# Kernel tuning notes

Measured on AMD Instinct MI355X. Metric: run time of the kernel, lower is better.

## Reference

```python
import jax, jax.numpy as jnp
import numpy as np

NEG = -9e8

def _leaky(x):
    return jax.nn.leaky_relu(x, 0.01)

def _gru(x, h, wih, whh, bih, bhh):
    # torch.nn.GRUCell math
    gi = x @ wih.T + bih
    gh = h @ whh.T + bhh
    ir, iz, inn = jnp.split(gi, 3, axis=-1)
    hr, hz, hn = jnp.split(gh, 3, axis=-1)
    r = jax.nn.sigmoid(ir + hr)
    z = jax.nn.sigmoid(iz + hz)
    n = jnp.tanh(inn + r * hn)
    return (1.0 - z) * n + z * h

def _gather(feat, idx):
    # feat [B,S,F], idx [B,S,K] -> [B,S,K,F]; -1 wraps to last row, masked later (same as torch)
    return jax.vmap(lambda f, i: f[i])(feat, idx)

def setup_inputs() -> dict:
    key = jax.random.key(0)
    ks = jax.random.split(key, 32)
    B, S, K, F_in, E, R = 32, 512, 21, 26, 256, 3
    amino_list = jax.random.uniform(ks[0], (B, S, F_in), dtype=jnp.float32)
    idx = jax.random.randint(ks[1], (B, S, K), 0, S, dtype=jnp.int32)
    pad = jax.random.uniform(ks[2], (B, S, K)) < 0.3
    amino_degree_list = jnp.where(pad, jnp.int32(-1), idx)
    # variable sequence lengths for mask
    lens = jax.random.randint(ks[3], (B,), S // 2, S + 1)
    amino_mask = (jnp.arange(S)[None, :] < lens[:, None]).astype(jnp.float32)
    s = 0.05
    d = dict(
        amino_list=amino_list,
        amino_degree_list=amino_degree_list,
        amino_mask=amino_mask,
        emb_W=jax.random.normal(ks[4], (E, F_in)) * s,
        emb_b=jax.random.normal(ks[5], (E,)) * s,
        neigh_W=jax.random.normal(ks[6], (E, F_in)) * s,
        neigh_b=jax.random.normal(ks[7], (E,)) * s,
        align_W=jax.random.normal(ks[8], (R, 1, 2 * E)) * s,
        align_b=jax.random.normal(ks[9], (R, 1)) * s,
        attend_W=jax.random.normal(ks[10], (R, E, E)) * s,
        attend_b=jax.random.normal(ks[11], (R, E)) * s,
        gru_wih=jax.random.normal(ks[12], (R, 3 * E, E)) * s,
        gru_whh=jax.random.normal(ks[13], (R, 3 * E, E)) * s,
        gru_bih=jax.random.normal(ks[14], (R, 3 * E)) * s,
        gru_bhh=jax.random.normal(ks[15], (R, 3 * E)) * s,
        seq_align_W=jax.random.normal(ks[16], (1, 2 * E)) * s,
        seq_align_b=jax.random.normal(ks[17], (1,)) * s,
        seq_attend_W=jax.random.normal(ks[18], (E, E)) * s,
        seq_attend_b=jax.random.normal(ks[19], (E,)) * s,
        sgru_wih=jax.random.normal(ks[20], (3 * E, E)) * s,
        sgru_whh=jax.random.normal(ks[21], (3 * E, E)) * s,
        sgru_bih=jax.random.normal(ks[22], (3 * E,)) * s,
        sgru_bhh=jax.random.normal(ks[23], (3 * E,)) * s,
    )
    return d

RADIUS = 3
T_STEPS = 2

def reference(amino_list, amino_degree_list, amino_mask,
              emb_W, emb_b, neigh_W, neigh_b,
              align_W, align_b, attend_W, attend_b,
              gru_wih, gru_whh, gru_bih, gru_bhh,
              seq_align_W, seq_align_b, seq_attend_W, seq_attend_b,
              sgru_wih, sgru_whh, sgru_bih, sgru_bhh):
    B, S, _ = amino_list.shape
    E = emb_W.shape[0]
    K = amino_degree_list.shape[-1]

    mask3 = amino_mask[:, :, None]                       # [B,S,1]
    amino_feature = _leaky(amino_list @ emb_W.T + emb_b)  # [B,S,E]

    attend_mask = (amino_degree_list != -1).astype(jnp.float32)[..., None]   # [B,S,K,1]
    softmax_mask = jnp.where(amino_degree_list == -1, NEG, 0.0)[..., None]   # [B,S,K,1]

    # first radius step: neighbors from raw one-hot features via neighbor_fc
    neighbor = _gather(amino_list, amino_degree_list)                 # [B,S,K,F_in]
    neighbor_feature = _leaky(neighbor @ neigh_W.T + neigh_b)         # [B,S,K,E]

    h = amino_feature.reshape(B * S, E)
    activated = None
    for d in range(RADIUS):
        if d == 0:
            nbr = neighbor_feature
            cur = amino_feature
        else:
            nbr = _gather(activated, amino_degree_list)               # [B,S,K,E]
            cur = activated
        cur_exp = jnp.broadcast_to(cur[:, :, None, :], (B, S, K, E))
        feat_align = jnp.concatenate([cur_exp, nbr], axis=-1)         # [B,S,K,2E]
        score = _leaky(feat_align @ align_W[d].T + align_b[d]) + softmax_mask
        attw = jax.nn.softmax(score, axis=-2) * attend_mask           # [B,S,K,1]
        nbr_t = nbr @ attend_W[d].T + attend_b[d]                     # [B,S,K,E]
        context = jax.nn.elu(jnp.sum(attw * nbr_t, axis=-2))          # [B,S,E]
        h = _gru(context.reshape(B * S, E), h, gru_wih[d], gru_whh[d], gru_bih[d], gru_bhh[d])
        activated = jax.nn.relu(h.reshape(B, S, E))

    seq_feature = jnp.sum(activated * mask3, axis=-2)                 # [B,E]
    act_mol = jax.nn.relu(seq_feature)
    seq_softmax_mask = jnp.where(mask3 == 0.0, NEG, 0.0)              # [B,S,1]

    act_seq = act_mol
    for _ in range(T_STEPS):
        mol_exp = jnp.broadcast_to(act_mol[:, None, :], (B, S, E))
        sa = jnp.concatenate([mol_exp, activated], axis=-1)           # [B,S,2E]
        score = _leaky(sa @ seq_align_W.T + seq_align_b) + seq_softmax_mask
        w = jax.nn.softmax(score, axis=-2) * mask3                    # [B,S,1]
        feat_t = activated @ seq_attend_W.T + seq_attend_b            # [B,S,E]
        seq_context = jax.nn.elu(jnp.sum(w * feat_t, axis=-2))        # [B,E]
        seq_feature = _gru(seq_context, seq_feature, sgru_wih, sgru_whh, sgru_bih, sgru_bhh)
        act_seq = jax.nn.relu(seq_feature)
    return act_seq
```

## Files before the change

kernel.cpp:

```cpp
#include <hip/hip_runtime.h>
#include <hip/hip_bf16.h>
#include <math.h>


#define NEGC (-9.0e8f)

typedef __attribute__((ext_vector_type(8))) short bf16x8;
typedef __attribute__((ext_vector_type(4))) float f32x4;

__device__ __forceinline__ ushort f2bf(float x) {
    union { float f; unsigned u; } v; v.f = x;
    unsigned r = v.u + 0x7FFF + ((v.u >> 16) & 1);
    return (ushort)(r >> 16);
}
__device__ __forceinline__ float bf2f(ushort u) {
    union { unsigned u; float f; } v; v.u = ((unsigned)u) << 16;
    return v.f;
}
__device__ __forceinline__ float sigm_fast(float x) {
    return 1.f / (1.f + __expf(-x));
}
__device__ __forceinline__ float tanh_fast(float x) {
    return 1.f - 2.f / (__expf(2.f * x) + 1.f);
}
__device__ __forceinline__ float elu_fast(float x) {
    return x > 0.f ? x : (__expf(x) - 1.f);
}

typedef const __attribute__((address_space(1))) void gvoid_t;
typedef __attribute__((address_space(3))) void lvoid_t;

__global__ __launch_bounds__(256) void cvt4_kernel(
    const float* __restrict__ s0, ushort* __restrict__ d0, int n0,
    const float* __restrict__ s1, ushort* __restrict__ d1, int n1,
    const float* __restrict__ s2, ushort* __restrict__ d2, int n2,
    const float* __restrict__ s3, ushort* __restrict__ d3, int n3)
{
    int i = blockIdx.x * 256 + threadIdx.x;
    const float* s; ushort* dst; int l;
    if (i < n0) { s = s0; dst = d0; l = i; }
    else if (i < n0 + n1) { s = s1; dst = d1; l = i - n0; }
    else if (i < n0 + n1 + n2) { s = s2; dst = d2; l = i - n0 - n1; }
    else if (i < n0 + n1 + n2 + n3) { s = s3; dst = d3; l = i - n0 - n1 - n2; }
    else return;
    float4 v = *reinterpret_cast<const float4*>(s + (size_t)l * 4);
    ushort4 o; o.x = f2bf(v.x); o.y = f2bf(v.y); o.z = f2bf(v.z); o.w = f2bf(v.w);
    *reinterpret_cast<ushort4*>(dst + (size_t)l * 4) = o;
}

__global__ __launch_bounds__(256) void gemm_dual_kernel(
    const ushort* __restrict__ A0, const ushort* __restrict__ W0,
    const float* __restrict__ b0, ushort* __restrict__ C0, int n0t,
    const ushort* __restrict__ A1, const ushort* __restrict__ W1,
    const float* __restrict__ b1, ushort* __restrict__ C1, int n1t,
    int K,
    const float* __restrict__ dw1, const float* __restrict__ dw2,
    float* __restrict__ dout1, float* __restrict__ dout2)
{
    __shared__ __align__(16) short As[128 * 32];
    __shared__ __align__(16) short Bs[128 * 32];
    int nwg = gridDim.x;
    int q = nwg >> 3;
    int flat = blockIdx.x;
    int sw = (flat & 7) * q + (flat >> 3);
    int tot = n0t + n1t;
    int bmi = sw / tot, bni = sw - bmi * tot;
    const ushort* A; const ushort* W; const float* bias; ushort* C; int N, bn;
    if (bni < n0t) { A = A0; W = W0; bias = b0; C = C0; N = n0t << 7; bn = bni << 7; }
    else { A = A1; W = W1; bias = b1; C = C1; N = n1t << 7; bn = (bni - n0t) << 7; }
    int bm = bmi << 7;

    int tid = threadIdx.x;
    int lane = tid & 63;
    int w = tid >> 6;
    int wr = w >> 1, wc = w & 1;
    bool dots = (dout1 != nullptr) && (bni == 0);

    f32x4 acc[4][4];
#pragma unroll
    for (int m = 0; m < 4; ++m)
#pragma unroll
        for (int n = 0; n < 4; ++n) acc[m][n] = (f32x4){0.f, 0.f, 0.f, 0.f};
    float p1 = 0.f, p2 = 0.f;

    for (int k0 = 0; k0 < K; k0 += 32) {
#pragma unroll
        for (int i = 0; i < 2; ++i) {
            int e = w * 1024 + i * 512 + lane * 8;
            int r = e >> 5, c = e & 31;
            const ushort* ga = A + (size_t)(bm + r) * K + (k0 + c);
            const ushort* gw = W + (size_t)(bn + r) * K + (k0 + c);
            __builtin_amdgcn_global_load_lds((gvoid_t*)ga, (lvoid_t*)&As[w * 1024 + i * 512], 16, 0, 0);
            __builtin_amdgcn_global_load_lds((gvoid_t*)gw, (lvoid_t*)&Bs[w * 1024 + i * 512], 16, 0, 0);
        }
        __syncthreads();
        bf16x8 af[4], bw[4];
        int ra = wr * 64 + (lane & 15);
        int rb = wc * 64 + (lane & 15);
        int kc = (lane >> 4) * 8;
#pragma unroll
        for (int m = 0; m < 4; ++m)
            af[m] = *reinterpret_cast<const bf16x8*>(&As[(ra + m * 16) * 32 + kc]);
#pragma unroll
        for (int n = 0; n < 4; ++n)
            bw[n] = *reinterpret_cast<const bf16x8*>(&Bs[(rb + n * 16) * 32 + kc]);
#pragma unroll
        for (int m = 0; m < 4; ++m)
#pragma unroll
            for (int n = 0; n < 4; ++n)
                acc[m][n] = __builtin_amdgcn_mfma_f32_16x16x32_bf16(af[m], bw[n], acc[m][n], 0, 0, 0);
        if (dots) {
            int drow = tid >> 1, kh = (tid & 1) << 4;
            const short* ar = &As[drow * 32 + kh];
#pragma unroll
            for (int c = 0; c < 16; ++c) {
                float av = bf2f((ushort)ar[c]);
                p1 = fmaf(av, dw1[k0 + kh + c], p1);
                if (dw2) p2 = fmaf(av, dw2[k0 + kh + c], p2);
            }
        }
        __syncthreads();
    }

    if (dots) {
        p1 += __shfl_xor(p1, 1);
        if (dw2) p2 += __shfl_xor(p2, 1);
        if ((tid & 1) == 0) {
            dout1[bm + (tid >> 1)] = p1;
            if (dw2) dout2[bm + (tid >> 1)] = p2;
        }
    }

    int cr0 = bm + wr * 64 + ((lane >> 4) * 4);
    int cc0 = bn + wc * 64 + (lane & 15);
#pragma unroll
    for (int n = 0; n < 4; ++n) {
        int col = cc0 + n * 16;
        float bv = bias[col];
#pragma unroll
        for (int m = 0; m < 4; ++m) {
            int row0 = cr0 + m * 16;
#pragma unroll
            for (int j = 0; j < 4; ++j) {
                float v = acc[m][n][j] + bv;
                C[(size_t)(row0 + j) * N + col] = f2bf(v);
            }
        }
    }
}

__global__ __launch_bounds__(512) void gru_fused_kernel(
    const ushort* __restrict__ ctx, const ushort* __restrict__ wih,
    const float* __restrict__ bih, const ushort* __restrict__ whh,
    const float* __restrict__ bhh,
    ushort* __restrict__ h_bf, ushort* __restrict__ act_bf)
{
    __shared__ __align__(16) short lds[32768];
    int flat = blockIdx.x;
    int sw = (flat & 7) * 32 + (flat >> 3);
    int bmi = sw >> 1, ct = sw & 1;
    int bm = bmi << 7;
    int tid = threadIdx.x;
    int lane = tid & 63;
    int w = tid >> 6;
    int wr = w >> 1, wc = w & 1;

    f32x4 acc[6][2][4];
#pragma unroll
    for (int qq = 0; qq < 6; ++qq)
#pragma unroll
        for (int m = 0; m < 2; ++m)
#pragma unroll
            for (int n = 0; n < 4; ++n) acc[qq][m][n] = (f32x4){0.f, 0.f, 0.f, 0.f};

    for (int k0 = 0; k0 < 256; k0 += 32) {
#pragma unroll
        for (int i = 0; i < 8; ++i) {
            int ch = i * 512 + tid;
            const ushort* src;
            if (ch < 512) {
                int r = ch >> 2, c = (ch & 3) << 3;
                src = ctx + (size_t)(bm + r) * 256 + k0 + c;
            } else if (ch < 1024) {
                int g = ch - 512;
                int r = g >> 2, c = (g & 3) << 3;
                src = h_bf + (size_t)(bm + r) * 256 + k0 + c;
            } else {
                int qw = (ch - 1024) >> 9;
                int g = (ch - 1024) & 511;
                int r = g >> 2, c = (g & 3) << 3;
                const ushort* wb = (qw < 3) ? wih : whh;
                int slice = (qw < 3) ? qw : qw - 3;
                src = wb + (size_t)(slice * 256 + ct * 128 + r) * 256 + k0 + c;
            }
            int chb = i * 512 + (tid & 0x1C0);
            __builtin_amdgcn_global_load_lds((gvoid_t*)src, (lvoid_t*)&lds[(size_t)chb * 8], 16, 0, 0);
        }
        __syncthreads();
        int rl = lane & 15;
        int kc = (lane >> 4) * 8;
        bf16x8 a_c[2], a_h[2];
#pragma unroll
        for (int m = 0; m < 2; ++m) {
            a_c[m] = *reinterpret_cast<const bf16x8*>(&lds[(wr * 32 + m * 16 + rl) * 32 + kc]);
            a_h[m] = *reinterpret_cast<const bf16x8*>(&lds[4096 + (wr * 32 + m * 16 + rl) * 32 + kc]);
        }
#pragma unroll
        for (int qq = 0; qq < 6; ++qq) {
            bf16x8 bw[4];
#pragma unroll
            for (int n = 0; n < 4; ++n)
                bw[n] = *reinterpret_cast<const bf16x8*>(
                    &lds[8192 + qq * 4096 + (wc * 64 + n * 16 + rl) * 32 + kc]);
#pragma unroll
            for (int m = 0; m < 2; ++m)
#pragma unroll
                for (int n = 0; n < 4; ++n)
                    acc[qq][m][n] = __builtin_amdgcn_mfma_f32_16x16x32_bf16(
                        (qq < 3) ? a_c[m] : a_h[m], bw[n], acc[qq][m][n], 0, 0, 0);
        }
        __syncthreads();
    }

#pragma unroll
    for (int n = 0; n < 4; ++n) {
        int col = ct * 128 + wc * 64 + n * 16 + (lane & 15);
        float bir = bih[col], biz = bih[256 + col], bin = bih[512 + col];
        float bhr = bhh[col], bhz = bhh[256 + col], bhn = bhh[512 + col];
#pragma unroll
        for (int m = 0; m < 2; ++m) {
            int row0 = bm + wr * 32 + m * 16 + ((lane >> 4) * 4);
#pragma unroll
            for (int j = 0; j < 4; ++j) {
                size_t idx = (size_t)(row0 + j) * 256 + col;
                float r = sigm_fast(acc[0][m][n][j] + bir + acc[3][m][n][j] + bhr);
                float z = sigm_fast(acc[1][m][n][j] + biz + acc[4][m][n][j] + bhz);
                float nn = tanh_fast(acc[2][m][n][j] + bin + r * (acc[5][m][n][j] + bhn));
                float hold = bf2f(h_bf[idx]);
                float hh = (1.f - z) * nn + z * hold;
                h_bf[idx] = f2bf(hh);
                act_bf[idx] = f2bf(fmaxf(hh, 0.f));
            }
        }
    }
}

__global__ __launch_bounds__(256) void embed_kernel(
    const float* __restrict__ amino, const float* __restrict__ embW,
    const float* __restrict__ embB, const float* __restrict__ neighW,
    const float* __restrict__ neighB,
    ushort* __restrict__ h_bf, ushort* __restrict__ nf_bf)
{
    const int FIN = 26, FPAD = 28, ROWS = 64;
    __shared__ __align__(16) float xs[ROWS][FPAD];
    int tid = threadIdx.x;
    float wE[FPAD], wN[FPAD];
#pragma unroll
    for (int f = 0; f < FIN; ++f) {
        wE[f] = embW[tid * FIN + f];
        wN[f] = neighW[tid * FIN + f];
    }
    wE[26] = wE[27] = wN[26] = wN[27] = 0.f;
    float b1 = embB[tid], b2 = neighB[tid];
    int row0 = blockIdx.x * ROWS;
    for (int idx = tid; idx < ROWS * FPAD; idx += 256) {
        int r = idx / FPAD, f = idx - r * FPAD;
        xs[r][f] = (f < FIN) ? amino[(size_t)(row0 + r) * FIN + f] : 0.f;
    }
    __syncthreads();
    for (int r = 0; r < ROWS; ++r) {
        const float4* x4 = reinterpret_cast<const float4*>(xs[r]);
        float a = b1, c = b2;
#pragma unroll
        for (int q = 0; q < 7; ++q) {
            float4 x = x4[q];
            a = fmaf(x.x, wE[4 * q], a);     c = fmaf(x.x, wN[4 * q], c);
            a = fmaf(x.y, wE[4 * q + 1], a); c = fmaf(x.y, wN[4 * q + 1], c);
            a = fmaf(x.z, wE[4 * q + 2], a); c = fmaf(x.z, wN[4 * q + 2], c);
            a = fmaf(x.w, wE[4 * q + 3], a); c = fmaf(x.w, wN[4 * q + 3], c);
        }
        a = a > 0.f ? a : 0.01f * a;
        c = c > 0.f ? c : 0.01f * c;
        size_t idx = (size_t)(row0 + r) * 256 + tid;
        h_bf[idx] = f2bf(a);
        nf_bf[idx] = f2bf(c);
    }
}

__global__ __launch_bounds__(256) void rowdots_bf16_kernel(
    const ushort* __restrict__ cur, const ushort* __restrict__ nbr,
    const float* __restrict__ alignW, float* __restrict__ ca, float* __restrict__ cb)
{
    int tid = threadIdx.x;
    int wv = tid >> 6, lane = tid & 63;
    size_t row = (size_t)blockIdx.x * 4 + wv;
    int e0 = lane * 4;
    ushort4 cv = *reinterpret_cast<const ushort4*>(cur + row * 256 + e0);
    ushort4 nv = *reinterpret_cast<const ushort4*>(nbr + row * 256 + e0);
    float4 w1 = *reinterpret_cast<const float4*>(alignW + e0);
    float4 w2 = *reinterpret_cast<const float4*>(alignW + 256 + e0);
    float p1 = bf2f(cv.x) * w1.x + bf2f(cv.y) * w1.y + bf2f(cv.z) * w1.z + bf2f(cv.w) * w1.w;
    float p2 = bf2f(nv.x) * w2.x + bf2f(nv.y) * w2.y + bf2f(nv.z) * w2.z + bf2f(nv.w) * w2.w;
#pragma unroll
    for (int off = 32; off > 0; off >>= 1) {
        p1 += __shfl_down(p1, off);
        p2 += __shfl_down(p2, off);
    }
    if (lane == 0) { ca[row] = p1; cb[row] = p2; }
}

__global__ __launch_bounds__(256) void attn_kernel(
    const int* __restrict__ deg, const float* __restrict__ ca,
    const float* __restrict__ cbrow, const ushort* __restrict__ act_t,
    const float* __restrict__ alignB, int d,
    ushort* __restrict__ context_bf, int S)
{
    const int KNB = 21;
    int raw = blockIdx.x;
    int bid = (raw & 7) * 512 + (raw >> 3);
    int bs0 = bid * 4;
    int b = bs0 >> 9;
    int tid = threadIdx.x;
    int wv = tid >> 6, lane = tid & 63;
    int bs = bs0 + wv;
    __shared__ float ss[4][KNB];
    __shared__ int   sj[4][KNB];
    if (lane < KNB) {
        int j = deg[bs * KNB + lane];
        float cbv = (j >= 0) ? cbrow[b * S + j] : 0.f;
        float sc = ca[bs] + cbv + alignB[d];
        sc = sc > 0.f ? sc : 0.01f * sc;
        if (j < 0) sc += NEGC;
        sj[wv][lane] = j;
        ss[wv][lane] = sc;
    }
    __syncthreads();
    float mx = -3.4e38f;
#pragma unroll
    for (int k = 0; k < KNB; ++k) mx = fmaxf(mx, ss[wv][k]);
    float se[KNB];
    float sum = 0.f;
#pragma unroll
    for (int k = 0; k < KNB; ++k) { se[k] = __expf(ss[wv][k] - mx); sum += se[k]; }
    float inv = 1.f / sum;
    const ushort* base = act_t + (size_t)b * S * 256 + lane * 4;
    float a0 = 0.f, a1 = 0.f, a2 = 0.f, a3 = 0.f;
#pragma unroll
    for (int k = 0; k < KNB; ++k) {
        int j = sj[wv][k];
        if (j >= 0) {
            ushort4 v = *reinterpret_cast<const ushort4*>(base + (size_t)j * 256);
            float wk = se[k];
            a0 = fmaf(wk, bf2f(v.x), a0);
            a1 = fmaf(wk, bf2f(v.y), a1);
            a2 = fmaf(wk, bf2f(v.z), a2);
            a3 = fmaf(wk, bf2f(v.w), a3);
        }
    }
    ushort4 o;
    o.x = f2bf(elu_fast(a0 * inv));
    o.y = f2bf(elu_fast(a1 * inv));
    o.z = f2bf(elu_fast(a2 * inv));
    o.w = f2bf(elu_fast(a3 * inv));
    *reinterpret_cast<ushort4*>(&context_bf[(size_t)bs * 256 + lane * 4]) = o;
}

__global__ __launch_bounds__(256) void seqpool_partial_kernel(
    const ushort* __restrict__ act, const float* __restrict__ mask,
    float* __restrict__ partial, int S, int CH)
{
    int bc = blockIdx.x;
    int NC = S / CH;
    int b = bc / NC, c = bc - b * NC;
    int tid = threadIdx.x;
    int s0 = c * CH;
    const ushort* ab = act + ((size_t)b * S + s0) * 256;
    const float* mb = mask + b * S + s0;
    float acc = 0.f;
    for (int s = 0; s < CH; ++s)
        acc = fmaf(bf2f(ab[(size_t)s * 256 + tid]), mb[s], acc);
    partial[(size_t)bc * 256 + tid] = acc;
}

__global__ __launch_bounds__(256) void seqpool_sm_kernel(
    const float* __restrict__ partial, const float* __restrict__ saW,
    const float* __restrict__ praw, const float* __restrict__ sab,
    const float* __restrict__ mask,
    float* __restrict__ seqfeat, float* __restrict__ wout, int NC, int S)
{
    int b = blockIdx.x, tid = threadIdx.x;
    int lane = tid & 63, wv = tid >> 6;
    __shared__ float red[4];
    __shared__ float sw[512];
    __shared__ float r1[4], r2[4];
    __shared__ float smd;
    float acc = 0.f;
    for (int c = 0; c < NC; ++c)
        acc += partial[((size_t)b * NC + c) * 256 + tid];
    seqfeat[b * 256 + tid] = acc;
    float am = fmaxf(acc, 0.f);
    float p = am * saW[tid];
#pragma unroll
    for (int off = 32; off > 0; off >>= 1) p += __shfl_down(p, off);
    if (lane == 0) red[wv] = p;
    __syncthreads();
    if (tid == 0) smd = red[0] + red[1] + red[2] + red[3];
    __syncthreads();
    float md = smd, sb = sab[0];
    float lm = -3.4e38f;
    for (int s = tid; s < S; s += 256) {
        float sc = md + praw[b * S + s] + sb;
        sc = sc > 0.f ? sc : 0.01f * sc;
        if (mask[b * S + s] == 0.f) sc += NEGC;
        sw[s] = sc;
        lm = fmaxf(lm, sc);
    }
#pragma unroll
    for (int off = 32; off > 0; off >>= 1) lm = fmaxf(lm, __shfl_down(lm, off));
    if (lane == 0) r1[wv] = lm;
    __syncthreads();
    float mx = fmaxf(fmaxf(r1[0], r1[1]), fmaxf(r1[2], r1[3]));
    float ls = 0.f;
    for (int s = tid; s < S; s += 256) {
        float e = __expf(sw[s] - mx);
        sw[s] = e * mask[b * S + s];
        ls += e;
    }
#pragma unroll
    for (int off = 32; off > 0; off >>= 1) ls += __shfl_down(ls, off);
    if (lane == 0) r2[wv] = ls;
    __syncthreads();
    float inv = 1.f / (r2[0] + r2[1] + r2[2] + r2[3]);
    for (int s = tid; s < S; s += 256)
        wout[b * S + s] = sw[s] * inv;
}

__global__ __launch_bounds__(256) void seqctx_partial_kernel(
    const float* __restrict__ w, const ushort* __restrict__ feat,
    float* __restrict__ partial, int S, int CH)
{
    int bc = blockIdx.x;
    int NC = S / CH;
    int b = bc / NC, c = bc - b * NC;
    int tid = threadIdx.x;
    int s0 = c * CH;
    const ushort* fb = feat + ((size_t)b * S + s0) * 256;
    const float* wb = w + b * S + s0;
    float acc = 0.f;
    for (int s = 0; s < CH; ++s)
        acc = fmaf(wb[s], bf2f(fb[(size_t)s * 256 + tid]), acc);
    partial[(size_t)bc * 256 + tid] = acc;
}

__global__ __launch_bounds__(256) void seqctx_combine_kernel(
    const float* __restrict__ partial, float* __restrict__ sctx, int NC)
{
    int b = blockIdx.x, tid = threadIdx.x;
    float acc = 0.f;
    for (int c = 0; c < NC; ++c)
        acc += partial[((size_t)b * NC + c) * 256 + tid];
    sctx[b * 256 + tid] = elu_fast(acc);
}

__global__ __launch_bounds__(256) void sgru_mm_kernel(
    const float* __restrict__ x, const float* __restrict__ hseq,
    const float* __restrict__ wih, const float* __restrict__ whh,
    const float* __restrict__ bih, const float* __restrict__ bhh,
    float* __restrict__ g, int full)
{
    int per_b = full ? 1536 : 768;
    int o = blockIdx.x * 4 + (threadIdx.x >> 6);
    int lane = threadIdx.x & 63;
    int b = o / per_b;
    int j = o - b * per_b;
    if (!full) j += 768;
    const float* src; const float* w; const float* bp; int jj;
    if (j < 768) { src = x + b * 256; w = wih; bp = bih; jj = j; }
    else         { src = hseq + b * 256; w = whh; bp = bhh; jj = j - 768; }
    float p = 0.f;
#pragma unroll
    for (int i = 0; i < 4; ++i) {
        int idx = lane + 64 * i;
        p = fmaf(src[idx], w[(size_t)jj * 256 + idx], p);
    }
#pragma unroll
    for (int off = 32; off > 0; off >>= 1) p += __shfl_down(p, off);
    if (lane == 0) g[b * 1536 + j] = p + bp[jj];
}

__global__ __launch_bounds__(256) void sgru_gate_kernel(
    const float* __restrict__ g, float* __restrict__ hseq, float* __restrict__ out)
{
    int b = blockIdx.x, e = threadIdx.x;
    const float* gr = g + b * 1536;
    float r = sigm_fast(gr[e] + gr[768 + e]);
    float z = sigm_fast(gr[256 + e] + gr[1024 + e]);
    float n = tanh_fast(gr[512 + e] + r * gr[1280 + e]);
    float hv = hseq[b * 256 + e];
    float hn = (1.f - z) * n + z * hv;
    hseq[b * 256 + e] = hn;
    out[b * 256 + e] = fmaxf(hn, 0.f);
}

extern "C" void kernel_launch(void* const* d_in, const int* in_sizes, int n_in,
                              void* d_out, int out_size, void* d_ws, size_t ws_size,
                              hipStream_t stream)
{
    const float* amino   = (const float*)d_in[0];
    const int*   deg     = (const int*)  d_in[1];
    const float* mask    = (const float*)d_in[2];
    const float* embW    = (const float*)d_in[3];
    const float* embB    = (const float*)d_in[4];
    const float* neighW  = (const float*)d_in[5];
    const float* neighB  = (const float*)d_in[6];
    const float* alignW  = (const float*)d_in[7];
    const float* alignB  = (const float*)d_in[8];
    const float* attendW = (const float*)d_in[9];
    const float* attendB = (const float*)d_in[10];
    const float* gruWih  = (const float*)d_in[11];
    const float* gruWhh  = (const float*)d_in[12];
    const float* gruBih  = (const float*)d_in[13];
    const float* gruBhh  = (const float*)d_in[14];
    const float* saW     = (const float*)d_in[15];
    const float* saB     = (const float*)d_in[16];
    const float* seqAttW = (const float*)d_in[17];
    const float* seqAttB = (const float*)d_in[18];
    const float* sWih    = (const float*)d_in[19];
    const float* sWhh    = (const float*)d_in[20];
    const float* sBih    = (const float*)d_in[21];
    const float* sBhh    = (const float*)d_in[22];
    float* out = (float*)d_out;

    const int B = 32, S = 512;
    const int BS = B * S;
    const size_t N1 = (size_t)BS * 256;
    const int CH = 32, NC = S / CH;

    ushort* h_bf   = (ushort*)d_ws;
    ushort* act_bf = h_bf + N1;
    ushort* nb_bf  = act_bf + N1;
    ushort* att_bf = nb_bf + N1;
    ushort* attW_bf = att_bf + N1;
    ushort* wih_bf  = attW_bf + 3 * 256 * 256;
    ushort* whh_bf  = wih_bf + 3 * 768 * 256;
    ushort* saW2_bf = whh_bf + 3 * 768 * 256;
    float* smalls = (float*)(saW2_bf + 256 * 256);
    float* ca   = smalls;
    float* cb   = ca + BS;
    float* scor = cb + BS;
    float* wbuf = scor + BS;
    float* seqf = wbuf + BS;
    float* sctx = seqf + B * 256;
    float* g    = sctx + B * 256;
    float* part = g + B * 1536;

    const int c0 = (3 * 256 * 256) / 4, c1 = (3 * 768 * 256) / 4,
              c2 = (3 * 768 * 256) / 4, c3 = (256 * 256) / 4;
    cvt4_kernel<<<(c0 + c1 + c2 + c3 + 255) / 256, 256, 0, stream>>>(
        attendW, attW_bf, c0, gruWih, wih_bf, c1, gruWhh, whh_bf, c2, seqAttW, saW2_bf, c3);

    embed_kernel<<<BS / 64, 256, 0, stream>>>(amino, embW, embB, neighW, neighB,
                                              h_bf, nb_bf);
    rowdots_bf16_kernel<<<BS / 4, 256, 0, stream>>>(h_bf, nb_bf, alignW, ca, cb);

    for (int d = 0; d < 3; ++d) {
        const ushort* nbr_bf = (d == 0) ? nb_bf : act_bf;
        gemm_dual_kernel<<<128 * 2, 256, 0, stream>>>(
            nbr_bf, attW_bf + d * 256 * 256, attendB + d * 256, att_bf, 2,
            (const ushort*)nullptr, (const ushort*)nullptr, (const float*)nullptr,
            (ushort*)nullptr, 0, 256,
            d == 0 ? (const float*)nullptr : alignW + d * 512,
            d == 0 ? (const float*)nullptr : alignW + d * 512 + 256,
            d == 0 ? (float*)nullptr : ca,
            d == 0 ? (float*)nullptr : cb);
        attn_kernel<<<BS / 4, 256, 0, stream>>>(deg, ca, cb, att_bf, alignB, d, nb_bf, S);
        gru_fused_kernel<<<128 * 2, 512, 0, stream>>>(
            nb_bf, wih_bf + d * 768 * 256, gruBih + d * 768,
            whh_bf + d * 768 * 256, gruBhh + d * 768, h_bf, act_bf);
    }

    seqpool_partial_kernel<<<B * NC, 256, 0, stream>>>(act_bf, mask, part, S, CH);
    gemm_dual_kernel<<<128 * 2, 256, 0, stream>>>(
        act_bf, saW2_bf, seqAttB, att_bf, 2,
        (const ushort*)nullptr, (const ushort*)nullptr, (const float*)nullptr,
        (ushort*)nullptr, 0, 256,
        saW + 256, (const float*)nullptr, scor, (float*)nullptr);
    seqpool_sm_kernel<<<B, 256, 0, stream>>>(part, saW, scor, saB, mask, seqf, wbuf, NC, S);
    seqctx_partial_kernel<<<B * NC, 256, 0, stream>>>(wbuf, att_bf, part, S, CH);
    seqctx_combine_kernel<<<B, 256, 0, stream>>>(part, sctx, NC);

    sgru_mm_kernel<<<B * 1536 / 4, 256, 0, stream>>>(sctx, seqf, sWih, sWhh, sBih, sBhh, g, 1);
    sgru_gate_kernel<<<B, 256, 0, stream>>>(g, seqf, out);
    sgru_mm_kernel<<<B * 768 / 4, 256, 0, stream>>>(sctx, seqf, sWih, sWhh, sBih, sBhh, g, 0);
    sgru_gate_kernel<<<B, 256, 0, stream>>>(g, seqf, out);
}
```

Before: 289.5 us.

## Retile GRU kernel to 64x64 blocks and fuse sequence GRU into one kernel

The per-layer GRU kernel moves from 128x128 tiles with 512 threads to 64x64 tiles with 256 threads, giving four times as many blocks. The hidden state is ping-ponged between two buffers so reads and writes never alias. The sequence-level combine, matvec and gate kernels for both GRU steps are merged into one per-batch kernel, which removes several launches. The trade-offs are more weight reloads per tile and a low-parallelism fused tail kernel with uncoalesced weight reads.

Measured after the change: 337.1 us. 16.4% more time.

```diff
diff --git a/kernel.cpp b/kernel.cpp
--- a/kernel.cpp
+++ b/kernel.cpp
@@ -149,52 +149,47 @@
     }
 }
 
-__global__ __launch_bounds__(512) void gru_fused_kernel(
+__global__ __launch_bounds__(256) void gru_fused_kernel(
     const ushort* __restrict__ ctx, const ushort* __restrict__ wih,
     const float* __restrict__ bih, const ushort* __restrict__ whh,
     const float* __restrict__ bhh,
-    ushort* __restrict__ h_bf, ushort* __restrict__ act_bf)
-{
-    __shared__ __align__(16) short lds[32768];
+    const ushort* __restrict__ h_in, ushort* __restrict__ h_out,
+    ushort* __restrict__ act_bf)
+{
+    __shared__ __align__(16) short lds[16384];
     int flat = blockIdx.x;
-    int sw = (flat & 7) * 32 + (flat >> 3);
-    int bmi = sw >> 1, ct = sw & 1;
-    int bm = bmi << 7;
+    int sw = (flat & 7) * 128 + (flat >> 3);
+    int bmi = sw >> 2, ct = sw & 3;
+    int bm = bmi << 6;
     int tid = threadIdx.x;
     int lane = tid & 63;
     int w = tid >> 6;
     int wr = w >> 1, wc = w & 1;
 
-    f32x4 acc[6][2][4];
+    f32x4 acc[6][2][2];
 #pragma unroll
     for (int qq = 0; qq < 6; ++qq)
 #pragma unroll
         for (int m = 0; m < 2; ++m)
 #pragma unroll
-            for (int n = 0; n < 4; ++n) acc[qq][m][n] = (f32x4){0.f, 0.f, 0.f, 0.f};
-
+            for (int n = 0; n < 2; ++n) acc[qq][m][n] = (f32x4){0.f, 0.f, 0.f, 0.f};
+
+    int srow = tid >> 2, scol = (tid & 3) << 3;
+    int ldst = (tid & 0xC0) * 8;
     for (int k0 = 0; k0 < 256; k0 += 32) {
-#pragma unroll
-        for (int i = 0; i < 8; ++i) {
-            int ch = i * 512 + tid;
-            const ushort* src;
-            if (ch < 512) {
-                int r = ch >> 2, c = (ch & 3) << 3;
-                src = ctx + (size_t)(bm + r) * 256 + k0 + c;
-            } else if (ch < 1024) {
-                int g = ch - 512;
-                int r = g >> 2, c = (g & 3) << 3;
-                src = h_bf + (size_t)(bm + r) * 256 + k0 + c;
-            } else {
-                int qw = (ch - 1024) >> 9;
-                int g = (ch - 1024) & 511;
-                int r = g >> 2, c = (g & 3) << 3;
-                const ushort* wb = (qw < 3) ? wih : whh;
-                int slice = (qw < 3) ? qw : qw - 3;
-                src = wb + (size_t)(slice * 256 + ct * 128 + r) * 256 + k0 + c;
+        {
+            const ushort* s0 = ctx  + (size_t)(bm + srow) * 256 + k0 + scol;
+            const ushort* s1 = h_in + (size_t)(bm + srow) * 256 + k0 + scol;
+            __builtin_amdgcn_global_load_lds((gvoid_t*)s0, (lvoid_t*)&lds[ldst], 16, 0, 0);
+            __builtin_amdgcn_global_load_lds((gvoid_t*)s1, (lvoid_t*)&lds[2048 + ldst], 16, 0, 0);
+#pragma unroll
+            for (int qq = 0; qq < 6; ++qq) {
+                const ushort* wb = (qq < 3) ? wih : whh;
+                int slice = (qq < 3) ? qq : qq - 3;
+                const ushort* sv = wb + (size_t)(slice * 256 + ct * 64 + srow) * 256 + k0 + scol;
+                __builtin_amdgcn_global_load_lds((gvoid_t*)sv,
+                    (lvoid_t*)&lds[(2 + qq) * 2048 + ldst], 16, 0, 0);
             }
-            int chb = i * 512 + (tid & 0x1C0);
-            __builtin_amdgcn_global_load_lds((gvoid_t*)src, (lvoid_t*)&lds[(size_t)chb * 8], 16, 0, 0);
         }
         __syncthreads();
         int rl = lane & 15;
@@ -203,19 +198,19 @@
 #pragma unroll
         for (int m = 0; m < 2; ++m) {
             a_c[m] = *reinterpret_cast<const bf16x8*>(&lds[(wr * 32 + m * 16 + rl) * 32 + kc]);
-            a_h[m] = *reinterpret_cast<const bf16x8*>(&lds[4096 + (wr * 32 + m * 16 + rl) * 32 + kc]);
+            a_h[m] = *reinterpret_cast<const bf16x8*>(&lds[2048 + (wr * 32 + m * 16 + rl) * 32 + kc]);
         }
 #pragma unroll
         for (int qq = 0; qq < 6; ++qq) {
-            bf16x8 bw[4];
-#pragma unroll
-            for (int n = 0; n < 4; ++n)
+            bf16x8 bw[2];
+#pragma unroll
+            for (int n = 0; n < 2; ++n)
                 bw[n] = *reinterpret_cast<const bf16x8*>(
-                    &lds[8192 + qq * 4096 + (wc * 64 + n * 16 + rl) * 32 + kc]);
+                    &lds[(2 + qq) * 2048 + (wc * 32 + n * 16 + rl) * 32 + kc]);
 #pragma unroll
             for (int m = 0; m < 2; ++m)
 #pragma unroll
-                for (int n = 0; n < 4; ++n)
+                for (int n = 0; n < 2; ++n)
                     acc[qq][m][n] = __builtin_amdgcn_mfma_f32_16x16x32_bf16(
                         (qq < 3) ? a_c[m] : a_h[m], bw[n], acc[qq][m][n], 0, 0, 0);
         }
@@ -223,8 +218,8 @@
     }
 
 #pragma unroll
-    for (int n = 0; n < 4; ++n) {
-        int col = ct * 128 + wc * 64 + n * 16 + (lane & 15);
+    for (int n = 0; n < 2; ++n) {
+        int col = ct * 64 + wc * 32 + n * 16 + (lane & 15);
         float bir = bih[col], biz = bih[256 + col], bin = bih[512 + col];
         float bhr = bhh[col], bhz = bhh[256 + col], bhn = bhh[512 + col];
 #pragma unroll
@@ -236,9 +231,9 @@
                 float r = sigm_fast(acc[0][m][n][j] + bir + acc[3][m][n][j] + bhr);
                 float z = sigm_fast(acc[1][m][n][j] + biz + acc[4][m][n][j] + bhz);
                 float nn = tanh_fast(acc[2][m][n][j] + bin + r * (acc[5][m][n][j] + bhn));
-                float hold = bf2f(h_bf[idx]);
+                float hold = bf2f(h_in[idx]);
                 float hh = (1.f - z) * nn + z * hold;
-                h_bf[idx] = f2bf(hh);
+                h_out[idx] = f2bf(hh);
                 act_bf[idx] = f2bf(fmaxf(hh, 0.f));
             }
         }
@@ -452,54 +447,63 @@
     partial[(size_t)bc * 256 + tid] = acc;
 }
 
-__global__ __launch_bounds__(256) void seqctx_combine_kernel(
-    const float* __restrict__ partial, float* __restrict__ sctx, int NC)
-{
+__global__ __launch_bounds__(256) void sgru_all_kernel(
+    const float* __restrict__ partial, int NC,
+    const float* __restrict__ seqf,
+    const float* __restrict__ sWih, const float* __restrict__ sWhh,
+    const float* __restrict__ sBih, const float* __restrict__ sBhh,
+    float* __restrict__ out)
+{
+    __shared__ float x[256];
+    __shared__ float hs[256];
     int b = blockIdx.x, tid = threadIdx.x;
     float acc = 0.f;
     for (int c = 0; c < NC; ++c)
         acc += partial[((size_t)b * NC + c) * 256 + tid];
-    sctx[b * 256 + tid] = elu_fast(acc);
-}
-
-__global__ __launch_bounds__(256) void sgru_mm_kernel(
-    const float* __restrict__ x, const float* __restrict__ hseq,
-    const float* __restrict__ wih, const float* __restrict__ whh,
-    const float* __restrict__ bih, const float* __restrict__ bhh,
-    float* __restrict__ g, int full)
-{
-    int per_b = full ? 1536 : 768;
-    int o = blockIdx.x * 4 + (threadIdx.x >> 6);
-    int lane = threadIdx.x & 63;
-    int b = o / per_b;
-    int j = o - b * per_b;
-    if (!full) j += 768;
-    const float* src; const float* w; const float* bp; int jj;
-    if (j < 768) { src = x + b * 256; w = wih; bp = bih; jj = j; }
-    else         { src = hseq + b * 256; w = whh; bp = bhh; jj = j - 768; }
-    float p = 0.f;
-#pragma unroll
-    for (int i = 0; i < 4; ++i) {
-        int idx = lane + 64 * i;
-        p = fmaf(src[idx], w[(size_t)jj * 256 + idx], p);
-    }
-#pragma unroll
-    for (int off = 32; off > 0; off >>= 1) p += __shfl_down(p, off);
-    if (lane == 0) g[b * 1536 + j] = p + bp[jj];
-}
-
-__global__ __launch_bounds__(256) void sgru_gate_kernel(
-    const float* __restrict__ g, float* __restrict__ hseq, float* __restrict__ out)
-{
-    int b = blockIdx.x, e = threadIdx.x;
-    const float* gr = g + b * 1536;
-    float r = sigm_fast(gr[e] + gr[768 + e]);
-    float z = sigm_fast(gr[256 + e] + gr[1024 + e]);
-    float n = tanh_fast(gr[512 + e] + r * gr[1280 + e]);
-    float hv = hseq[b * 256 + e];
-    float hn = (1.f - z) * n + z * hv;
-    hseq[b * 256 + e] = hn;
-    out[b * 256 + e] = fmaxf(hn, 0.f);
+    x[tid] = elu_fast(acc);
+    hs[tid] = seqf[b * 256 + tid];
+    __syncthreads();
+
+    float gi[3];
+#pragma unroll
+    for (int q = 0; q < 3; ++q) {
+        const float* wr_ = sWih + (size_t)(q * 256 + tid) * 256;
+        float p = 0.f;
+        for (int k = 0; k < 256; k += 4) {
+            float4 wv = *reinterpret_cast<const float4*>(wr_ + k);
+            p = fmaf(x[k], wv.x, p);
+            p = fmaf(x[k + 1], wv.y, p);
+            p = fmaf(x[k + 2], wv.z, p);
+            p = fmaf(x[k + 3], wv.w, p);
+        }
+        gi[q] = p + sBih[q * 256 + tid];
+    }
+
+    float hn = 0.f;
+    for (int t = 0; t < 2; ++t) {
+        float gh[3];
+#pragma unroll
+        for (int q = 0; q < 3; ++q) {
+            const float* wr_ = sWhh + (size_t)(q * 256 + tid) * 256;
+            float p = 0.f;
+            for (int k = 0; k < 256; k += 4) {
+                float4 wv = *reinterpret_cast<const float4*>(wr_ + k);
+                p = fmaf(hs[k], wv.x, p);
+                p = fmaf(hs[k + 1], wv.y, p);
+                p = fmaf(hs[k + 2], wv.z, p);
+                p = fmaf(hs[k + 3], wv.w, p);
+            }
+            gh[q] = p + sBhh[q * 256 + tid];
+        }
+        float r = sigm_fast(gi[0] + gh[0]);
+        float z = sigm_fast(gi[1] + gh[1]);
+        float n = tanh_fast(gi[2] + r * gh[2]);
+        hn = (1.f - z) * n + z * hs[tid];
+        __syncthreads();
+        hs[tid] = hn;
+        __syncthreads();
+    }
+    out[b * 256 + tid] = fmaxf(hn, 0.f);
 }
 
 extern "C" void kernel_launch(void* const* d_in, const int* in_sizes, int n_in,
@@ -536,8 +540,9 @@
     const size_t N1 = (size_t)BS * 256;
     const int CH = 32, NC = S / CH;
 
-    ushort* h_bf   = (ushort*)d_ws;
-    ushort* act_bf = h_bf + N1;
+    ushort* hA     = (ushort*)d_ws;
+    ushort* hB     = hA + N1;
+    ushort* act_bf = hB + N1;
     ushort* nb_bf  = act_bf + N1;
     ushort* att_bf = nb_bf + N1;
     ushort* attW_bf = att_bf + N1;
@@ -550,9 +555,7 @@
     float* scor = cb + BS;
     float* wbuf = scor + BS;
     float* seqf = wbuf + BS;
-    float* sctx = seqf + B * 256;
-    float* g    = sctx + B * 256;
-    float* part = g + B * 1536;
+    float* part = seqf + B * 256;
 
     const int c0 = (3 * 256 * 256) / 4, c1 = (3 * 768 * 256) / 4,
               c2 = (3 * 768 * 256) / 4, c3 = (256 * 256) / 4;
@@ -560,11 +563,13 @@
         attendW, attW_bf, c0, gruWih, wih_bf, c1, gruWhh, whh_bf, c2, seqAttW, saW2_bf, c3);
 
     embed_kernel<<<BS / 64, 256, 0, stream>>>(amino, embW, embB, neighW, neighB,
-                                              h_bf, nb_bf);
-    rowdots_bf16_kernel<<<BS / 4, 256, 0, stream>>>(h_bf, nb_bf, alignW, ca, cb);
+                                              hA, nb_bf);
+    rowdots_bf16_kernel<<<BS / 4, 256, 0, stream>>>(hA, nb_bf, alignW, ca, cb);
 
     for (int d = 0; d < 3; ++d) {
         const ushort* nbr_bf = (d == 0) ? nb_bf : act_bf;
+        const ushort* h_in  = (d & 1) ? hB : hA;
+        ushort*       h_out = (d & 1) ? hA : hB;
         gemm_dual_kernel<<<128 * 2, 256, 0, stream>>>(
             nbr_bf, attW_bf + d * 256 * 256, attendB + d * 256, att_bf, 2,
             (const ushort*)nullptr, (const ushort*)nullptr, (const float*)nullptr,
@@ -574,9 +579,9 @@
             d == 0 ? (float*)nullptr : ca,
             d == 0 ? (float*)nullptr : cb);
         attn_kernel<<<BS / 4, 256, 0, stream>>>(deg, ca, cb, att_bf, alignB, d, nb_bf, S);
-        gru_fused_kernel<<<128 * 2, 512, 0, stream>>>(
+        gru_fused_kernel<<<1024, 256, 0, stream>>>(
             nb_bf, wih_bf + d * 768 * 256, gruBih + d * 768,
-            whh_bf + d * 768 * 256, gruBhh + d * 768, h_bf, act_bf);
+            whh_bf + d * 768 * 256, gruBhh + d * 768, h_in, h_out, act_bf);
     }
 
     seqpool_partial_kernel<<<B * NC, 256, 0, stream>>>(act_bf, mask, part, S, CH);
@@ -587,10 +592,5 @@
         saW + 256, (const float*)nullptr, scor, (float*)nullptr);
     seqpool_sm_kernel<<<B, 256, 0, stream>>>(part, saW, scor, saB, mask, seqf, wbuf, NC, S);
     seqctx_partial_kernel<<<B * NC, 256, 0, stream>>>(wbuf, att_bf, part, S, CH);
-    seqctx_combine_kernel<<<B, 256, 0, stream>>>(part, sctx, NC);
-
-    sgru_mm_kernel<<<B * 1536 / 4, 256, 0, stream>>>(sctx, seqf, sWih, sWhh, sBih, sBhh, g, 1);
-    sgru_gate_kernel<<<B, 256, 0, stream>>>(g, seqf, out);
-    sgru_mm_kernel<<<B * 768 / 4, 256, 0, stream>>>(sctx, seqf, sWih, sWhh, sBih, sBhh, g, 0);
-    sgru_gate_kernel<<<B, 256, 0, stream>>>(g, seqf, out);
-}
+    sgru_all_kernel<<<B, 256, 0, stream>>>(part, NC, seqf, sWih, sWhh, sBih, sBhh, out);
+}
```
